# Optimization experiments

Measured on AMD Instinct MI355X. Metric: run time of the kernel, lower is better.

Reference implementation:

```python
import jax, jax.numpy as jnp
import numpy as np

N = 100000       # nodes
E = 640000       # edges
G = 2048         # graphs in batch
IN_C, HID, NCLS = 3, 128, 4


def setup_inputs() -> dict:
    key = jax.random.key(0)
    ks = jax.random.split(key, 16)
    x = jax.random.normal(ks[0], (N, IN_C), dtype=jnp.float32)
    edge_index = jax.random.randint(ks[1], (2, E), 0, N, dtype=jnp.int64)
    batch = jnp.sort(jax.random.randint(ks[2], (N,), 0, G, dtype=jnp.int64))
    def glorot(k, shape):
        lim = np.sqrt(6.0 / (shape[0] + shape[1])).astype(np.float32)
        return jax.random.uniform(k, shape, jnp.float32, -lim, lim)
    return {
        "x": x, "edge_index": edge_index, "batch": batch,
        "W1": glorot(ks[3], (IN_C, HID)), "b1": jnp.zeros((HID,), jnp.float32),
        "W2": glorot(ks[4], (HID, HID)),  "b2": jnp.zeros((HID,), jnp.float32),
        "W3": glorot(ks[5], (HID, HID)),  "b3": jnp.zeros((HID,), jnp.float32),
        "W4": glorot(ks[6], (HID, HID)),  "b4": jnp.zeros((HID,), jnp.float32),
        "Wfc": glorot(ks[7], (HID, NCLS)), "bfc": jnp.zeros((NCLS,), jnp.float32),
    }


def _gcn_norm(edge_index):
    # Add self loops, then symmetric normalization D^{-1/2} (A+I) D^{-1/2}.
    loop = jnp.arange(N, dtype=edge_index.dtype)
    row = jnp.concatenate([edge_index[0], loop])  # source
    col = jnp.concatenate([edge_index[1], loop])  # target (aggregation side)
    deg = jax.ops.segment_sum(jnp.ones_like(col, dtype=jnp.float32), col,
                              num_segments=N)
    dinv = jnp.where(deg > 0, jax.lax.rsqrt(deg), 0.0)
    norm = dinv[row] * dinv[col]  # [E+N]
    return row, col, norm


def _gcn_layer(x, W, b, row, col, norm):
    h = x @ W                                 # [N, out]
    msg = h[row] * norm[:, None]              # gather + scale, [E+N, out]
    out = jax.ops.segment_sum(msg, col, num_segments=N)
    return out + b


def reference(x, edge_index, batch, W1, b1, W2, b2, W3, b3, W4, b4, Wfc, bfc):
    row, col, norm = _gcn_norm(edge_index)
    h = jax.nn.relu(_gcn_layer(x, W1, b1, row, col, norm))
    h = jax.nn.relu(_gcn_layer(h, W2, b2, row, col, norm))
    h = jax.nn.relu(_gcn_layer(h, W3, b3, row, col, norm))
    h = jax.nn.relu(_gcn_layer(h, W4, b4, row, col, norm))
    # global mean pool over graphs
    sums = jax.ops.segment_sum(h, batch, num_segments=G)           # [G, HID]
    cnt = jax.ops.segment_sum(jnp.ones((N,), jnp.float32), batch,
                              num_segments=G)
    pooled = sums / jnp.maximum(cnt, 1.0)[:, None]
    return pooled @ Wfc + bfc                                      # [G, NCLS]
```

## Files before the change

### kernel.cpp

```cpp
#include <hip/hip_runtime.h>
#include <hip/hip_bf16.h>

#define N_NODES  100000
#define N_EDGES  640000
#define N_GRAPHS 2048
#define HID      128
#define NB_SCAN  391
#define TILE     16
#define LDW      136

typedef _Float16 half_t;
typedef __attribute__((ext_vector_type(4))) _Float16 half4;
typedef __attribute__((ext_vector_type(8))) _Float16 half8;
typedef __attribute__((ext_vector_type(4))) float floatx4;

__global__ void k_prep(const int* __restrict__ col, int* __restrict__ deg,
                       const float* __restrict__ x, float4* __restrict__ xp,
                       half4* __restrict__ xh,
                       const float* __restrict__ W2, const float* __restrict__ W3,
                       const float* __restrict__ W4, half_t* __restrict__ Wt) {
    int idx = blockIdx.x * 256 + threadIdx.x;
    if (idx < N_EDGES) atomicAdd(&deg[col[idx]], 1);
    if (idx < N_NODES) {
        float x0 = x[idx * 3 + 0], x1 = x[idx * 3 + 1], x2 = x[idx * 3 + 2];
        xp[idx] = make_float4(x0, x1, x2, 0.f);
        half4 hv;
        hv.x = (half_t)x0; hv.y = (half_t)x1; hv.z = (half_t)x2; hv.w = (half_t)0.f;
        xh[idx] = hv;
    }
    if (idx < 3 * 128 * 128) {
        int l = idx >> 14;
        int e = idx & 16383;
        int cin = e >> 7, cout = e & 127;
        const float* W = (l == 0) ? W2 : ((l == 1) ? W3 : W4);
        Wt[l * 16384 + cout * 128 + cin] = (half_t)W[cin * 128 + cout];
    }
}

__global__ void k_scan1(const int* __restrict__ deg, int* __restrict__ row_ptr,
                        int* __restrict__ bsum, float* __restrict__ dinv) {
    __shared__ int s[256];
    int tid = threadIdx.x;
    int i = blockIdx.x * 256 + tid;
    int d = (i < N_NODES) ? deg[i] : 0;
    if (i < N_NODES) dinv[i] = rsqrtf((float)(d + 1));
    s[tid] = d;
    __syncthreads();
    for (int off = 1; off < 256; off <<= 1) {
        int v = (tid >= off) ? s[tid - off] : 0;
        __syncthreads();
        s[tid] += v;
        __syncthreads();
    }
    if (i < N_NODES) row_ptr[i] = s[tid] - d;
    if (tid == 255) bsum[blockIdx.x] = s[255];
}

__global__ void k_scan3(int* __restrict__ row_ptr, const int* __restrict__ bsum) {
    __shared__ int sred[256];
    int t = threadIdx.x, bid = blockIdx.x;
    int partial = 0;
    if (t < bid) partial += bsum[t];
    if (t + 256 < bid) partial += bsum[t + 256];
    sred[t] = partial;
    __syncthreads();
    for (int s = 128; s > 0; s >>= 1) {
        if (t < s) sred[t] += sred[t + s];
        __syncthreads();
    }
    int add = sred[0];
    int i = bid * 256 + t;
    if (i < N_NODES) row_ptr[i] += add;
    if (i == N_NODES) row_ptr[N_NODES] = N_EDGES;
}

__global__ void k_scatter(const int* __restrict__ row, const int* __restrict__ col,
                          const int* __restrict__ row_ptr, int* __restrict__ cursor,
                          const float* __restrict__ dinv, int2* __restrict__ epair) {
    int e = blockIdx.x * blockDim.x + threadIdx.x;
    if (e >= N_EDGES) return;
    int c = col[e];
    int r = row[e];
    int p = row_ptr[c] + atomicAdd(&cursor[c], 1);
    epair[p] = make_int2(r, __float_as_int(dinv[r] * dinv[c]));
}

__global__ __launch_bounds__(256) void k_aggx_fc1(const float4* __restrict__ xp,
                                                  const half4* __restrict__ xh,
                                                  const int* __restrict__ row_ptr,
                                                  const int2* __restrict__ epair,
                                                  const float* __restrict__ dinv,
                                                  const float* __restrict__ W1,
                                                  const float* __restrict__ b1,
                                                  half_t* __restrict__ h) {
    __shared__ float sax[256][3];
    int t = threadIdx.x;
    int nb = blockIdx.x * 256;
    int i = nb + t;
    if (i < N_NODES) {
        float di = dinv[i];
        float sw = di * di;
        float4 xv = xp[i];
        float a0 = sw * xv.x, a1 = sw * xv.y, a2 = sw * xv.z;
        int s = row_ptr[i], e = row_ptr[i + 1];
        int k = s;
        for (; k + 4 <= e; k += 4) {
            int2 pr[4];
#pragma unroll
            for (int r = 0; r < 4; r++) pr[r] = epair[k + r];
            half4 bx[4];
#pragma unroll
            for (int r = 0; r < 4; r++) bx[r] = xh[pr[r].x];
#pragma unroll
            for (int r = 0; r < 4; r++) {
                float w = __int_as_float(pr[r].y);
                a0 += w * (float)bx[r].x;
                a1 += w * (float)bx[r].y;
                a2 += w * (float)bx[r].z;
            }
        }
        for (; k < e; k++) {
            int2 pr = epair[k];
            float w = __int_as_float(pr.y);
            half4 bx = xh[pr.x];
            a0 += w * (float)bx.x;
            a1 += w * (float)bx.y;
            a2 += w * (float)bx.z;
        }
        sax[t][0] = a0; sax[t][1] = a1; sax[t][2] = a2;
    }
    __syncthreads();
    int cq = t & 31, g8 = t >> 5;
    const float4* W14 = (const float4*)W1;
    float4 w0 = W14[cq], w1 = W14[32 + cq], w2 = W14[64 + cq];
    float4 bb = ((const float4*)b1)[cq];
    for (int pass = 0; pass < 32; pass++) {
        int local = pass * 8 + g8;
        int node = nb + local;
        if (node >= N_NODES) break;
        float x0 = sax[local][0], x1 = sax[local][1], x2 = sax[local][2];
        half4 o;
        o.x = (half_t)fmaxf(bb.x + x0 * w0.x + x1 * w1.x + x2 * w2.x, 0.f);
        o.y = (half_t)fmaxf(bb.y + x0 * w0.y + x1 * w1.y + x2 * w2.y, 0.f);
        o.z = (half_t)fmaxf(bb.z + x0 * w0.z + x1 * w1.z + x2 * w2.z, 0.f);
        o.w = (half_t)fmaxf(bb.w + x0 * w0.w + x1 * w1.w + x2 * w2.w, 0.f);
        ((half4*)h)[(size_t)node * 32 + cq] = o;
    }
}

__global__ __launch_bounds__(256, 8) void k_agg_mm(const half_t* __restrict__ h_in,
                                                   const int* __restrict__ row_ptr,
                                                   const int2* __restrict__ epair,
                                                   const float* __restrict__ dinv,
                                                   const half_t* __restrict__ Wt,
                                                   const float* __restrict__ b,
                                                   half_t* __restrict__ h_out) {
    __shared__ __align__(16) half_t gs[TILE][LDW];
    int tid = threadIdx.x;
    int n0 = blockIdx.x * TILE;
    int lane16 = tid & 15;
    int gidx = tid >> 4;
    const half8* h8 = (const half8*)h_in;

    {
        int i = n0 + gidx;
        float di = dinv[i];
        float sw = di * di;
        half8 v = h8[(size_t)i * 16 + lane16];
        float acc[8];
#pragma unroll
        for (int c = 0; c < 8; c++) acc[c] = sw * (float)v[c];
        int s = row_ptr[i], e = row_ptr[i + 1];
        if (s < e) {
            int em1 = e - 1;
            int2 p0 = epair[s];
            int k1 = min(s + 1, em1);
            int2 p1 = epair[k1];
            float w0 = __int_as_float(p0.y);
            float w1 = (s + 1 < e) ? __int_as_float(p1.y) : 0.f;
            half8 u0 = h8[(size_t)p0.x * 16 + lane16];
            half8 u1 = h8[(size_t)p1.x * 16 + lane16];
            for (int k = s; k < e; k += 2) {
                int k2 = min(k + 2, em1);
                int k3 = min(k + 3, em1);
                int2 p2 = epair[k2];
                int2 p3 = epair[k3];
                float w2 = (k + 2 < e) ? __int_as_float(p2.y) : 0.f;
                float w3 = (k + 3 < e) ? __int_as_float(p3.y) : 0.f;
                half8 m0 = h8[(size_t)p2.x * 16 + lane16];
                half8 m1 = h8[(size_t)p3.x * 16 + lane16];
#pragma unroll
                for (int c = 0; c < 8; c++) acc[c] += w0 * (float)u0[c] + w1 * (float)u1[c];
                u0 = m0; u1 = m1; w0 = w2; w1 = w3;
            }
        }
        half8 av;
#pragma unroll
        for (int c = 0; c < 8; c++) av[c] = (half_t)acc[c];
        *(half8*)(&gs[gidx][lane16 * 8]) = av;
    }
    __syncthreads();

    int wv = tid >> 6;
    int ln = tid & 15;
    int q  = (tid >> 4) & 3;
    int cbase = wv * 32;
    floatx4 C[2];
#pragma unroll
    for (int t = 0; t < 2; t++) {
        float bn = b[cbase + t * 16 + ln];
        C[t].x = bn; C[t].y = bn; C[t].z = bn; C[t].w = bn;
    }
#pragma unroll
    for (int kq = 0; kq < 4; kq++) {
        half8 a = *(const half8*)(&gs[ln][kq * 32 + q * 8]);
#pragma unroll
        for (int t = 0; t < 2; t++) {
            half8 bf = *(const half8*)(Wt + (size_t)(cbase + t * 16 + ln) * 128 + kq * 32 + q * 8);
            C[t] = __builtin_amdgcn_mfma_f32_16x16x32_f16(a, bf, C[t], 0, 0, 0);
        }
    }

    __syncthreads();
#pragma unroll
    for (int t = 0; t < 2; t++) {
#pragma unroll
        for (int reg = 0; reg < 4; reg++) {
            float dv = (reg == 0) ? C[t].x : (reg == 1) ? C[t].y : (reg == 2) ? C[t].z : C[t].w;
            gs[q * 4 + reg][cbase + t * 16 + ln] = (half_t)fmaxf(dv, 0.f);
        }
    }
    __syncthreads();
    {
        int r0 = tid >> 4;
        int c0 = tid & 15;
        int4* dst = (int4*)(h_out + (size_t)(n0 + r0) * 128);
        const int4* srcp = (const int4*)(&gs[r0][0]);
        dst[c0] = srcp[c0];
    }
}

__global__ __launch_bounds__(128) void k_pool_final(const half_t* __restrict__ h,
                                                    const int* __restrict__ batch,
                                                    const float* __restrict__ Wfc,
                                                    const float* __restrict__ bfc,
                                                    float* __restrict__ out) {
    __shared__ float sred[8][128];
    __shared__ float red[128][4];
    __shared__ int sb_s, eb_s;
    int g = blockIdx.x, t = threadIdx.x;
    if (t == 0) {
        int lo = 0, hi = N_NODES;
        while (lo < hi) { int mid = (lo + hi) >> 1; if (batch[mid] < g) lo = mid + 1; else hi = mid; }
        sb_s = lo;
        hi = N_NODES;
        while (lo < hi) { int mid = (lo + hi) >> 1; if (batch[mid] < g + 1) lo = mid + 1; else hi = mid; }
        eb_s = lo;
    }
    __syncthreads();
    int sb = sb_s, eb = eb_s;
    int lane16 = t & 15, slot = t >> 4;
    const half8* h8 = (const half8*)h;
    float acc[8];
#pragma unroll
    for (int c = 0; c < 8; c++) acc[c] = 0.f;
    for (int n = sb + slot; n < eb; n += 8) {
        half8 v = h8[(size_t)n * 16 + lane16];
#pragma unroll
        for (int c = 0; c < 8; c++) acc[c] += (float)v[c];
    }
#pragma unroll
    for (int c = 0; c < 8; c++) sred[slot][lane16 * 8 + c] = acc[c];
    __syncthreads();
    float pv = 0.f;
#pragma unroll
    for (int s2 = 0; s2 < 8; s2++) pv += sred[s2][t];
    float inv = 1.0f / fmaxf((float)(eb - sb), 1.0f);
    float v = pv * inv;
    float4 w = ((const float4*)Wfc)[t];
    red[t][0] = v * w.x; red[t][1] = v * w.y; red[t][2] = v * w.z; red[t][3] = v * w.w;
    __syncthreads();
    for (int s = 64; s > 0; s >>= 1) {
        if (t < s) {
            red[t][0] += red[t + s][0];
            red[t][1] += red[t + s][1];
            red[t][2] += red[t + s][2];
            red[t][3] += red[t + s][3];
        }
        __syncthreads();
    }
    if (t < 4) out[g * 4 + t] = red[0][t] + bfc[t];
}

extern "C" void kernel_launch(void* const* d_in, const int* in_sizes, int n_in,
                              void* d_out, int out_size, void* d_ws, size_t ws_size,
                              hipStream_t stream) {
    const float* x     = (const float*)d_in[0];
    const int*   ei    = (const int*)d_in[1];
    const int*   row   = ei;
    const int*   col   = ei + N_EDGES;
    const int*   batch = (const int*)d_in[2];
    const float* W1 = (const float*)d_in[3];
    const float* b1 = (const float*)d_in[4];
    const float* W2 = (const float*)d_in[5];
    const float* b2 = (const float*)d_in[6];
    const float* W3 = (const float*)d_in[7];
    const float* b3 = (const float*)d_in[8];
    const float* W4 = (const float*)d_in[9];
    const float* b4 = (const float*)d_in[10];
    const float* Wfc = (const float*)d_in[11];
    const float* bfc = (const float*)d_in[12];
    float* out = (float*)d_out;

    char* ws = (char*)d_ws;
    size_t off = 0;
    auto take = [&](size_t bytes) -> char* {
        char* p = ws + off;
        off = (off + bytes + 255) & ~(size_t)255;
        return p;
    };
    int*    deg     = (int*)take(N_NODES * 4);
    int*    cursor  = (int*)take(N_NODES * 4);
    size_t  zspan   = (size_t)((char*)cursor + N_NODES * 4 - (char*)deg);
    int*    row_ptr = (int*)take((N_NODES + 1) * 4);
    int*    bsum    = (int*)take(512 * 4);
    float*  dinv    = (float*)take(N_NODES * 4);
    float4* xp      = (float4*)take((size_t)N_NODES * 16);
    half4*  xh      = (half4*)take((size_t)N_NODES * 8);
    int2*   epair   = (int2*)take((size_t)N_EDGES * 8);
    half_t* wt16    = (half_t*)take((size_t)3 * 128 * 128 * 2);
    half_t* bufA    = (half_t*)take((size_t)N_NODES * 128 * 2);
    half_t* bufB    = (half_t*)take((size_t)N_NODES * 128 * 2);

    hipMemsetAsync(deg, 0, zspan, stream);

    k_prep<<<(N_EDGES + 255) / 256, 256, 0, stream>>>(col, deg, x, xp, xh, W2, W3, W4, wt16);
    k_scan1<<<NB_SCAN, 256, 0, stream>>>(deg, row_ptr, bsum, dinv);
    k_scan3<<<NB_SCAN, 256, 0, stream>>>(row_ptr, bsum);
    k_scatter<<<(N_EDGES + 255) / 256, 256, 0, stream>>>(row, col, row_ptr, cursor,
                                                         dinv, epair);
    k_aggx_fc1<<<NB_SCAN, 256, 0, stream>>>(xp, xh, row_ptr, epair, dinv, W1, b1, bufA);

    const int NBF = N_NODES / TILE;
    k_agg_mm<<<NBF, 256, 0, stream>>>(bufA, row_ptr, epair, dinv, wt16,         b2, bufB);
    k_agg_mm<<<NBF, 256, 0, stream>>>(bufB, row_ptr, epair, dinv, wt16 + 16384, b3, bufA);
    k_agg_mm<<<NBF, 256, 0, stream>>>(bufA, row_ptr, epair, dinv, wt16 + 32768, b4, bufB);

    k_pool_final<<<N_GRAPHS, 128, 0, stream>>>(bufB, batch, Wfc, bfc, out);
}
```

Measured before the change: 312.8 us.

## Process nodes in degree-sorted order to balance aggregation work across lanes

Builds a degree histogram and a counting-sort permutation of nodes by in-degree (capped at 32 bins), then has the first-layer aggregation and the three aggregate+matmul kernels process nodes in that permuted order, writing results back to original node positions. This groups nodes of similar degree into the same wavefront/tile so lanes finish their edge loops together and divergence from the random degree distribution drops. It adds two small kernels, an extra indirection load per node, and scattered output rows, which can reduce write coalescing and locality.

```diff
diff --git a/kernel.cpp b/kernel.cpp
--- a/kernel.cpp
+++ b/kernel.cpp
@@ -8,6 +8,7 @@
 #define NB_SCAN  391
 #define TILE     16
 #define LDW      136
+#define NBIN     32
 
 typedef _Float16 half_t;
 typedef __attribute__((ext_vector_type(4))) _Float16 half4;
@@ -38,14 +39,18 @@
 }
 
 __global__ void k_scan1(const int* __restrict__ deg, int* __restrict__ row_ptr,
-                        int* __restrict__ bsum, float* __restrict__ dinv) {
+                        int* __restrict__ bsum, float* __restrict__ dinv,
+                        int* __restrict__ dhist) {
     __shared__ int s[256];
+    __shared__ int hh[NBIN];
     int tid = threadIdx.x;
     int i = blockIdx.x * 256 + tid;
     int d = (i < N_NODES) ? deg[i] : 0;
     if (i < N_NODES) dinv[i] = rsqrtf((float)(d + 1));
     s[tid] = d;
-    __syncthreads();
+    if (tid < NBIN) hh[tid] = 0;
+    __syncthreads();
+    if (i < N_NODES) atomicAdd(&hh[min(d, NBIN - 1)], 1);
     for (int off = 1; off < 256; off <<= 1) {
         int v = (tid >= off) ? s[tid - off] : 0;
         __syncthreads();
@@ -54,6 +59,36 @@
     }
     if (i < N_NODES) row_ptr[i] = s[tid] - d;
     if (tid == 255) bsum[blockIdx.x] = s[255];
+    if (tid < NBIN && hh[tid] > 0) atomicAdd(&dhist[tid], hh[tid]);
+}
+
+__global__ void k_dscan(int* __restrict__ dhist) {
+    if (threadIdx.x == 0) {
+        int run = 0;
+        for (int b = 0; b < NBIN; b++) { int c = dhist[b]; dhist[b] = run; run += c; }
+    }
+}
+
+__global__ void k_dperm(const int* __restrict__ deg, const int* __restrict__ dbase,
+                        int* __restrict__ dcur, int* __restrict__ perm) {
+    __shared__ int hcnt[NBIN];
+    __shared__ int hbase[NBIN];
+    int t = threadIdx.x;
+    int i = blockIdx.x * 256 + t;
+    if (t < NBIN) hcnt[t] = 0;
+    __syncthreads();
+    int bin = 0, rank = 0;
+    if (i < N_NODES) {
+        bin = min(deg[i], NBIN - 1);
+        rank = atomicAdd(&hcnt[bin], 1);
+    }
+    __syncthreads();
+    if (t < NBIN) {
+        int c = hcnt[t];
+        hbase[t] = (c > 0) ? atomicAdd(&dcur[t], c) : 0;
+    }
+    __syncthreads();
+    if (i < N_NODES) perm[dbase[bin] + hbase[bin] + rank] = i;
 }
 
 __global__ void k_scan3(int* __restrict__ row_ptr, const int* __restrict__ bsum) {
@@ -90,6 +125,7 @@
                                                   const int* __restrict__ row_ptr,
                                                   const int2* __restrict__ epair,
                                                   const float* __restrict__ dinv,
+                                                  const int* __restrict__ perm,
                                                   const float* __restrict__ W1,
                                                   const float* __restrict__ b1,
                                                   half_t* __restrict__ h) {
@@ -98,11 +134,12 @@
     int nb = blockIdx.x * 256;
     int i = nb + t;
     if (i < N_NODES) {
-        float di = dinv[i];
+        int node = perm[i];
+        float di = dinv[node];
         float sw = di * di;
-        float4 xv = xp[i];
+        float4 xv = xp[node];
         float a0 = sw * xv.x, a1 = sw * xv.y, a2 = sw * xv.z;
-        int s = row_ptr[i], e = row_ptr[i + 1];
+        int s = row_ptr[node], e = row_ptr[node + 1];
         int k = s;
         for (; k + 4 <= e; k += 4) {
             int2 pr[4];
@@ -136,15 +173,16 @@
     float4 bb = ((const float4*)b1)[cq];
     for (int pass = 0; pass < 32; pass++) {
         int local = pass * 8 + g8;
-        int node = nb + local;
-        if (node >= N_NODES) break;
+        int slot = nb + local;
+        if (slot >= N_NODES) break;
+        int pn = perm[slot];
         float x0 = sax[local][0], x1 = sax[local][1], x2 = sax[local][2];
         half4 o;
         o.x = (half_t)fmaxf(bb.x + x0 * w0.x + x1 * w1.x + x2 * w2.x, 0.f);
         o.y = (half_t)fmaxf(bb.y + x0 * w0.y + x1 * w1.y + x2 * w2.y, 0.f);
         o.z = (half_t)fmaxf(bb.z + x0 * w0.z + x1 * w1.z + x2 * w2.z, 0.f);
         o.w = (half_t)fmaxf(bb.w + x0 * w0.w + x1 * w1.w + x2 * w2.w, 0.f);
-        ((half4*)h)[(size_t)node * 32 + cq] = o;
+        ((half4*)h)[(size_t)pn * 32 + cq] = o;
     }
 }
 
@@ -152,6 +190,7 @@
                                                    const int* __restrict__ row_ptr,
                                                    const int2* __restrict__ epair,
                                                    const float* __restrict__ dinv,
+                                                   const int* __restrict__ perm,
                                                    const half_t* __restrict__ Wt,
                                                    const float* __restrict__ b,
                                                    half_t* __restrict__ h_out) {
@@ -163,14 +202,14 @@
     const half8* h8 = (const half8*)h_in;
 
     {
-        int i = n0 + gidx;
-        float di = dinv[i];
+        int node = perm[n0 + gidx];
+        float di = dinv[node];
         float sw = di * di;
-        half8 v = h8[(size_t)i * 16 + lane16];
+        half8 v = h8[(size_t)node * 16 + lane16];
         float acc[8];
 #pragma unroll
         for (int c = 0; c < 8; c++) acc[c] = sw * (float)v[c];
-        int s = row_ptr[i], e = row_ptr[i + 1];
+        int s = row_ptr[node], e = row_ptr[node + 1];
         if (s < e) {
             int em1 = e - 1;
             int2 p0 = epair[s];
@@ -234,7 +273,8 @@
     {
         int r0 = tid >> 4;
         int c0 = tid & 15;
-        int4* dst = (int4*)(h_out + (size_t)(n0 + r0) * 128);
+        int pn = perm[n0 + r0];
+        int4* dst = (int4*)(h_out + (size_t)pn * 128);
         const int4* srcp = (const int4*)(&gs[r0][0]);
         dst[c0] = srcp[c0];
     }
@@ -321,10 +361,13 @@
     };
     int*    deg     = (int*)take(N_NODES * 4);
     int*    cursor  = (int*)take(N_NODES * 4);
-    size_t  zspan   = (size_t)((char*)cursor + N_NODES * 4 - (char*)deg);
+    int*    dhist   = (int*)take(2 * NBIN * 4);
+    int*    dcur    = dhist + NBIN;
+    size_t  zspan   = (size_t)((char*)(dhist + 2 * NBIN) - (char*)deg);
     int*    row_ptr = (int*)take((N_NODES + 1) * 4);
     int*    bsum    = (int*)take(512 * 4);
     float*  dinv    = (float*)take(N_NODES * 4);
+    int*    perm    = (int*)take(N_NODES * 4);
     float4* xp      = (float4*)take((size_t)N_NODES * 16);
     half4*  xh      = (half4*)take((size_t)N_NODES * 8);
     int2*   epair   = (int2*)take((size_t)N_EDGES * 8);
@@ -335,16 +378,18 @@
     hipMemsetAsync(deg, 0, zspan, stream);
 
     k_prep<<<(N_EDGES + 255) / 256, 256, 0, stream>>>(col, deg, x, xp, xh, W2, W3, W4, wt16);
-    k_scan1<<<NB_SCAN, 256, 0, stream>>>(deg, row_ptr, bsum, dinv);
+    k_scan1<<<NB_SCAN, 256, 0, stream>>>(deg, row_ptr, bsum, dinv, dhist);
+    k_dscan<<<1, 64, 0, stream>>>(dhist);
+    k_dperm<<<NB_SCAN, 256, 0, stream>>>(deg, dhist, dcur, perm);
     k_scan3<<<NB_SCAN, 256, 0, stream>>>(row_ptr, bsum);
     k_scatter<<<(N_EDGES + 255) / 256, 256, 0, stream>>>(row, col, row_ptr, cursor,
                                                          dinv, epair);
-    k_aggx_fc1<<<NB_SCAN, 256, 0, stream>>>(xp, xh, row_ptr, epair, dinv, W1, b1, bufA);
+    k_aggx_fc1<<<NB_SCAN, 256, 0, stream>>>(xp, xh, row_ptr, epair, dinv, perm, W1, b1, bufA);
 
     const int NBF = N_NODES / TILE;
-    k_agg_mm<<<NBF, 256, 0, stream>>>(bufA, row_ptr, epair, dinv, wt16,         b2, bufB);
-    k_agg_mm<<<NBF, 256, 0, stream>>>(bufB, row_ptr, epair, dinv, wt16 + 16384, b3, bufA);
-    k_agg_mm<<<NBF, 256, 0, stream>>>(bufA, row_ptr, epair, dinv, wt16 + 32768, b4, bufB);
+    k_agg_mm<<<NBF, 256, 0, stream>>>(bufA, row_ptr, epair, dinv, perm, wt16,         b2, bufB);
+    k_agg_mm<<<NBF, 256, 0, stream>>>(bufB, row_ptr, epair, dinv, perm, wt16 + 16384, b3, bufA);
+    k_agg_mm<<<NBF, 256, 0, stream>>>(bufA, row_ptr, epair, dinv, perm, wt16 + 32768, b4, bufB);
 
     k_pool_final<<<N_GRAPHS, 128, 0, stream>>>(bufB, batch, Wfc, bfc, out);
 }
```

Result: slower. 322.8 us (+3.2%).
